# Kernel optimization log

Hardware: AMD Instinct MI355X
Metric: run time of the kernel (lower is better)

## Reference

```python
import jax, jax.numpy as jnp
import numpy as np

PENALTY = -100.0  # reset penalty used by the torch module


def log_g(x):
    # torch: where(x >= 0, log(relu(x) + 0.5), -softplus(-x))
    return jnp.where(x >= 0, jnp.log(jax.nn.relu(x) + 0.5), -jax.nn.softplus(-x))


def setup_inputs() -> dict:
    key = jax.random.key(0)
    k1, k2, k3 = jax.random.split(key, 3)
    B, S, D = 4, 8192, 1024
    x = jax.random.normal(k1, (B, S, D), dtype=jnp.float32)
    W = jax.random.normal(k2, (D, 2 * D), dtype=jnp.float32) * (1.0 / np.sqrt(D))
    input_ids = jax.random.randint(k3, (B, S), 0, 32000, dtype=jnp.int64)
    return {"x": x, "W": W, "input_ids": input_ids}


def reference(x, W, input_ids):
    # x: [B,S,D], W: [D,2D] (to_hidden_and_gate, no bias), proj_out=False -> Identity
    hg = jnp.einsum("bsd,de->bse", x, W)            # [B,S,2D]
    hidden, gate = jnp.split(hg, 2, axis=-1)          # each [B,S,D]

    pad_mask = input_ids == 0                         # [B,S]

    log_coeffs = -jax.nn.softplus(gate)               # log(1 - z)
    log_z = -jax.nn.softplus(-gate)                   # log z
    log_values = log_z + log_g(hidden)                # log(z * h_tilde)

    # reset at positions following a pad token (shifted mask)
    reset = jnp.pad(pad_mask[:, :-1], ((0, 0), (1, 0)))[:, :, None]  # [B,S,1]

    lc = jnp.where(reset, PENALTY, log_coeffs)
    a_star = jnp.cumsum(lc, axis=1)
    lv = jnp.where(reset, PENALTY, log_values)
    log_h = a_star + jax.lax.cumlogsumexp(lv - a_star, axis=1)
    out = jnp.exp(log_h)                              # [B,S,D]

    next_prev_hidden = jnp.where(pad_mask[:, -1:, None], 0.0, out[:, -1:])
    return out, next_prev_hidden
```

## Files before the change

### kernel.cpp

```cpp
#include <hip/hip_runtime.h>
#include <hip/hip_fp16.h>
#include <math.h>

#define S_LEN 8192
#define D_DIM 1024
#define B_DIM 4
#define M_DIM (B_DIM * S_LEN)
#define BSD   ((size_t)M_DIM * D_DIM)
#define CHN   (B_DIM * D_DIM)
#define CHUNK 64
#define NCH   (S_LEN / CHUNK)

typedef _Float16 f16x8 __attribute__((ext_vector_type(8)));
typedef __attribute__((ext_vector_type(4))) float f32x4;
typedef unsigned int u32;

__device__ __forceinline__ u32 pk2h(float a, float b) {
    auto h = __builtin_amdgcn_cvt_pkrtz(a, b);
    u32 r; __builtin_memcpy(&r, &h, 4); return r;
}

__device__ __forceinline__ void gload16(const void* g, void* l) {
    __builtin_amdgcn_global_load_lds(
        (const __attribute__((address_space(1))) u32*)g,
        (__attribute__((address_space(3))) u32*)l,
        16, 0, 0);
}

__global__ __launch_bounds__(256) void w_to_f16t(
    const float* __restrict__ W, unsigned short* __restrict__ Wt)
{
    __shared__ float T[64][65];
    const int t  = threadIdx.x;
    const int n0 = (int)blockIdx.x * 64;
    const int k0 = (int)blockIdx.y * 64;
    #pragma unroll
    for (int p = 0; p < 4; ++p) {
        int u = p * 256 + t;
        int r = u >> 4, c4 = (u & 15) * 4;
        float4 v = *(const float4*)&W[(size_t)(k0 + r) * 2048 + n0 + c4];
        T[r][c4 + 0] = v.x; T[r][c4 + 1] = v.y;
        T[r][c4 + 2] = v.z; T[r][c4 + 3] = v.w;
    }
    __syncthreads();
    #pragma unroll
    for (int p = 0; p < 2; ++p) {
        int u = p * 256 + t;
        int n = u >> 3, kc = (u & 7) * 8;
        u32 out[4];
        #pragma unroll
        for (int j = 0; j < 4; ++j)
            out[j] = pk2h(T[kc + 2 * j][n], T[kc + 2 * j + 1][n]);
        *(uint4*)&Wt[(size_t)(n0 + n) * 1024 + k0 + kc] = *(uint4*)out;
    }
}

__global__ __launch_bounds__(256) void xw_prep(
    const float* __restrict__ x, unsigned short* __restrict__ xh,
    const float* __restrict__ W, unsigned short* __restrict__ Wt)
{
    const int bx = (int)blockIdx.x;
    if (bx < 16384) {
        int tid = bx * 256 + threadIdx.x;
        int m  = tid >> 7;
        int cg = tid & 127;
        const float4* src = (const float4*)&x[(size_t)m * 1024 + cg * 8];
        float4 v0 = src[0], v1 = src[1];
        u32 o[4] = { pk2h(v0.x, v0.y), pk2h(v0.z, v0.w),
                     pk2h(v1.x, v1.y), pk2h(v1.z, v1.w) };
        int j   = cg & 7;
        int cgd = (cg & ~7) | (j ^ (m & 7));
        *(uint4*)&xh[(size_t)m * 1024 + cgd * 8] = *(uint4*)o;
        return;
    }
    __shared__ float T[64][65];
    const int wb = bx - 16384;
    const int t  = threadIdx.x;
    const int n0 = (wb & 31) * 64;
    const int k0 = (wb >> 5) * 64;
    #pragma unroll
    for (int p = 0; p < 4; ++p) {
        int u = p * 256 + t;
        int r = u >> 4, c4 = (u & 15) * 4;
        float4 v = *(const float4*)&W[(size_t)(k0 + r) * 2048 + n0 + c4];
        T[r][c4 + 0] = v.x; T[r][c4 + 1] = v.y;
        T[r][c4 + 2] = v.z; T[r][c4 + 3] = v.w;
    }
    __syncthreads();
    #pragma unroll
    for (int p = 0; p < 2; ++p) {
        int u = p * 256 + t;
        int n = u >> 3, kc = (u & 7) * 8;
        u32 out[4];
        #pragma unroll
        for (int j = 0; j < 4; ++j)
            out[j] = pk2h(T[kc + 2 * j][n], T[kc + 2 * j + 1][n]);
        *(uint4*)&Wt[(size_t)(n0 + n) * 1024 + k0 + kc] = *(uint4*)out;
    }
}

__global__ __launch_bounds__(512, 2) void gemm_8p(
    const unsigned short* __restrict__ xh, const unsigned short* __restrict__ Wt,
    const int* __restrict__ ids, u32* __restrict__ P,
    float* __restrict__ Cp, float* __restrict__ Lp)
{
    __shared__ __align__(16) unsigned short Ah[2 * 256 * 64];
    __shared__ __align__(16) unsigned short Bt[2 * 256 * 64];

    const int t    = threadIdx.x;
    const int lane = t & 63;
    const int wid  = t >> 6;
    const int wm   = wid >> 2;
    const int wd   = wid & 3;

    const int lin  = (int)blockIdx.x;
    const int xcd  = lin & 7;
    const int slot = lin >> 3;
    const int m0   = (xcd * 16 + (slot >> 3)) * 256;
    const int c0   = (slot & 7) * 128;

    f32x4 accH[8][2], accG[8][2];
    #pragma unroll
    for (int i = 0; i < 8; ++i)
        #pragma unroll
        for (int j = 0; j < 2; ++j) {
            accH[i][j] = (f32x4)0.0f;
            accG[i][j] = (f32x4)0.0f;
        }

    auto stageA = [&](int kb, int buf, int half) {
        char* Ad = (char*)Ah + (buf << 15) + (half << 14);
        #pragma unroll
        for (int i = 0; i < 2; ++i) {
            int sl  = i * 512 + t;
            int row = half * 128 + (sl >> 3);
            int c   = sl & 7;
            const unsigned short* src =
                xh + ((size_t)(m0 + row) << 10) + kb + (c << 3);
            gload16(src, Ad + (size_t)sl * 16);
        }
    };
    auto stageB = [&](int kb, int buf, int half) {
        char* Bd = (char*)Bt + (buf << 15) + (half << 14);
        #pragma unroll
        for (int i = 0; i < 2; ++i) {
            int sl  = i * 512 + t;
            int col = sl >> 3;
            int kc  = (sl & 7) ^ (col & 7);
            const unsigned short* src =
                Wt + ((size_t)(half * 1024 + c0 + col) << 10) + kb + (kc << 3);
            gload16(src, Bd + (size_t)sl * 16);
        }
    };

    auto readA = [&](const char* Ab, int kk, f16x8 a[8]) {
        int chunk = kk * 4 + (lane >> 4);
        #pragma unroll
        for (int mf = 0; mf < 8; ++mf) {
            int row = wm * 128 + mf * 16 + (lane & 15);
            a[mf] = *(const f16x8*)(Ab + row * 128 + ((chunk ^ (row & 7)) << 4));
        }
    };
    auto readB = [&](const char* Bb, int kk, int hg, f16x8 b[2]) {
        int chunk = kk * 4 + (lane >> 4);
        #pragma unroll
        for (int df = 0; df < 2; ++df) {
            int col = wd * 32 + df * 16 + (lane & 15);
            b[df] = *(const f16x8*)(Bb + (hg * 128 + col) * 128
                                       + ((chunk ^ (col & 7)) << 4));
        }
    };

    #define MMA_CLUSTER(ACC, AV, BV)                                       \
        __builtin_amdgcn_s_setprio(1);                                     \
        _Pragma("unroll")                                                  \
        for (int mf = 0; mf < 8; ++mf)                                     \
            _Pragma("unroll")                                              \
            for (int df = 0; df < 2; ++df)                                 \
                ACC[mf][df] = __builtin_amdgcn_mfma_f32_16x16x32_f16(      \
                    AV[mf], BV[df], ACC[mf][df], 0, 0, 0);                 \
        __builtin_amdgcn_s_setprio(0);

    stageA(0, 0, 0); stageA(0, 0, 1); stageB(0, 0, 0); stageB(0, 0, 1);
    asm volatile("s_waitcnt vmcnt(0)" ::: "memory");
    __builtin_amdgcn_sched_barrier(0);
    __builtin_amdgcn_s_barrier();

    for (int tt = 0; tt < 16; ++tt) {
        const int buf   = tt & 1;
        const int kbn   = (tt + 1) << 6;
        const bool more = tt < 15;
        const char* Ab = (const char*)Ah + (buf << 15);
        const char* Bb = (const char*)Bt + (buf << 15);
        f16x8 a0[8], a1[8], bh0[2], bg0[2], bh1[2], bg1[2];

        readA(Ab, 0, a0); readB(Bb, 0, 0, bh0);
        if (more) { stageA(kbn, buf ^ 1, 0); stageA(kbn, buf ^ 1, 1); }
        asm volatile("s_waitcnt lgkmcnt(0)" ::: "memory");
        __builtin_amdgcn_sched_barrier(0);
        readB(Bb, 0, 1, bg0);
        __builtin_amdgcn_sched_barrier(0);
        MMA_CLUSTER(accH, a0, bh0)

        asm volatile("s_waitcnt lgkmcnt(0)" ::: "memory");
        __builtin_amdgcn_sched_barrier(0);
        readA(Ab, 1, a1); readB(Bb, 1, 0, bh1);
        if (more) { stageB(kbn, buf ^ 1, 0); stageB(kbn, buf ^ 1, 1); }
        __builtin_amdgcn_sched_barrier(0);
        MMA_CLUSTER(accG, a0, bg0)

        asm volatile("s_waitcnt lgkmcnt(0)" ::: "memory");
        __builtin_amdgcn_sched_barrier(0);
        readB(Bb, 1, 1, bg1);
        __builtin_amdgcn_sched_barrier(0);
        MMA_CLUSTER(accH, a1, bh1)

        asm volatile("s_waitcnt lgkmcnt(0)" ::: "memory");
        __builtin_amdgcn_sched_barrier(0);
        MMA_CLUSTER(accG, a1, bg1)
        if (more) {
            asm volatile("s_waitcnt vmcnt(0)" ::: "memory");
            __builtin_amdgcn_sched_barrier(0);
            __builtin_amdgcn_s_barrier();
        }
    }
    #undef MMA_CLUSTER

    __builtin_amdgcn_s_barrier();
    float* Caff = (float*)Ah;

    #pragma unroll
    for (int mf = 0; mf < 8; ++mf) {
        int mbase = m0 + wm * 128 + mf * 16 + (lane >> 4) * 4;
        float Cr[2] = {1.0f, 1.0f};
        float Lr[2] = {0.0f, 0.0f};
        #pragma unroll
        for (int r = 0; r < 4; ++r) {
            int m = mbase + r;
            int b = m >> 13;
            int s = m & 8191;
            bool reset = (s > 0) && (ids[b * S_LEN + s - 1] == 0);
            #pragma unroll
            for (int df = 0; df < 2; ++df) {
                int d = c0 + wd * 32 + df * 16 + (lane & 15);
                float hid = accH[mf][df][r];
                float g   = accG[mf][df][r];
                float eg  = __expf(-g);
                float z   = 1.0f / (1.0f + eg);
                float c   = eg * z;
                float gt  = (hid >= 0.0f) ? (hid + 0.5f)
                                          : 1.0f / (1.0f + __expf(-hid));
                float v   = z * gt;
                if (reset) { c = 0.0f; v = 0.0f; }
                __half2 h2 = __floats2half2_rn(c, v);
                u32 packed;
                __builtin_memcpy(&packed, &h2, 4);
                P[(size_t)m * D_DIM + d] = packed;
                Lr[df] = fmaf(c, Lr[df], v);
                Cr[df] *= c;
            }
        }
        int rq = wm * 32 + mf * 4 + (lane >> 4);
        #pragma unroll
        for (int df = 0; df < 2; ++df) {
            int col = wd * 32 + df * 16 + (lane & 15);
            Caff[(rq * 128 + col) * 2 + 0] = Cr[df];
            Caff[(rq * 128 + col) * 2 + 1] = Lr[df];
        }
    }
    __builtin_amdgcn_s_barrier();
    {
        int sc  = t >> 7;
        int col = t & 127;
        float C = 1.0f, L = 0.0f;
        #pragma unroll
        for (int q = 0; q < 16; ++q) {
            int rq = sc * 16 + q;
            float cq = Caff[(rq * 128 + col) * 2 + 0];
            float lq = Caff[(rq * 128 + col) * 2 + 1];
            L = fmaf(cq, L, lq);
            C *= cq;
        }
        int m    = m0 + sc * 64;
        int b    = m >> 13;
        int cidx = (m & 8191) >> 6;
        int ch   = (b << 10) | (c0 + col);
        Cp[cidx * CHN + ch] = C;
        Lp[cidx * CHN + ch] = L;
    }
}

__global__ __launch_bounds__(256, 3) void gemm_fb(
    const float* __restrict__ x, const unsigned short* __restrict__ Wt,
    const int* __restrict__ ids, u32* __restrict__ P)
{
    __shared__ __align__(16) unsigned short Ah[128 * 64];
    __shared__ __align__(16) unsigned short Bt[2 * 64 * 64];

    const int t    = threadIdx.x;
    const int lane = t & 63;
    const int wid  = t >> 6;
    const int wm   = wid >> 1;
    const int wd   = wid & 1;

    const int lin  = (int)blockIdx.y * (int)gridDim.x + (int)blockIdx.x;
    const int xcd  = lin & 7;
    const int slot = lin >> 3;
    const int m0   = (xcd * 32 + (slot >> 4)) * 128;
    const int c0   = (slot & 15) * 64;

    f32x4 accH[4][2], accG[4][2];
    #pragma unroll
    for (int i = 0; i < 4; ++i)
        #pragma unroll
        for (int j = 0; j < 2; ++j) {
            accH[i][j] = (f32x4)0.0f;
            accG[i][j] = (f32x4)0.0f;
        }

    for (int kb = 0; kb < 1024; kb += 64) {
        __syncthreads();
        #pragma unroll
        for (int i = 0; i < 4; ++i) {
            int slotb = wid * 256 + i * 64;
            int sl  = slotb + lane;
            int hg  = sl >> 9;
            int col = (sl >> 3) & 63;
            int kc  = (sl & 7) ^ (col & 7);
            const unsigned short* src =
                Wt + ((size_t)(hg * 1024 + c0 + col) << 10) + kb + (kc << 3);
            gload16(src, (char*)Bt + (size_t)slotb * 16);
        }
        #pragma unroll
        for (int p = 0; p < 8; ++p) {
            int s   = p * 256 + t;
            int row = s >> 4;
            int c4  = s & 15;
            float4 v = *(const float4*)&x[(size_t)(m0 + row) * 1024 + kb + c4 * 4];
            uint2 h;
            h.x = pk2h(v.x, v.y);
            h.y = pk2h(v.z, v.w);
            int byte = row * 128 + ((((c4 >> 1) ^ (row & 7))) << 4) + ((c4 & 1) << 3);
            *(uint2*)((char*)Ah + byte) = h;
        }
        __syncthreads();
        #pragma unroll
        for (int kk = 0; kk < 2; ++kk) {
            f16x8 bh[2], bg[2];
            #pragma unroll
            for (int df = 0; df < 2; ++df) {
                int col = wd * 32 + df * 16 + (lane & 15);
                int chunk = kk * 4 + (lane >> 4);
                int byte = col * 128 + ((chunk ^ (col & 7)) << 4);
                bh[df] = *(const f16x8*)((const char*)Bt + byte);
                bg[df] = *(const f16x8*)((const char*)Bt + 8192 + byte);
            }
            #pragma unroll
            for (int mf = 0; mf < 4; ++mf) {
                int row = wm * 64 + mf * 16 + (lane & 15);
                int chunk = kk * 4 + (lane >> 4);
                int byte = row * 128 + ((chunk ^ (row & 7)) << 4);
                f16x8 a = *(const f16x8*)((const char*)Ah + byte);
                #pragma unroll
                for (int df = 0; df < 2; ++df) {
                    accH[mf][df] = __builtin_amdgcn_mfma_f32_16x16x32_f16(
                        a, bh[df], accH[mf][df], 0, 0, 0);
                    accG[mf][df] = __builtin_amdgcn_mfma_f32_16x16x32_f16(
                        a, bg[df], accG[mf][df], 0, 0, 0);
                }
            }
        }
    }

    #pragma unroll
    for (int mf = 0; mf < 4; ++mf) {
        int mbase = m0 + wm * 64 + mf * 16 + (lane >> 4) * 4;
        #pragma unroll
        for (int r = 0; r < 4; ++r) {
            int m = mbase + r;
            int b = m >> 13;
            int s = m & 8191;
            bool reset = (s > 0) && (ids[b * S_LEN + s - 1] == 0);
            #pragma unroll
            for (int df = 0; df < 2; ++df) {
                int d = c0 + wd * 32 + df * 16 + (lane & 15);
                float hid = accH[mf][df][r];
                float g   = accG[mf][df][r];
                float eg  = __expf(-g);
                float z   = 1.0f / (1.0f + eg);
                float c   = eg * z;
                float gt  = (hid >= 0.0f) ? (hid + 0.5f)
                                          : 1.0f / (1.0f + __expf(-hid));
                float v   = z * gt;
                if (reset) { c = 0.0f; v = 0.0f; }
                __half2 h2 = __floats2half2_rn(c, v);
                u32 packed;
                __builtin_memcpy(&packed, &h2, 4);
                P[(size_t)m * D_DIM + d] = packed;
            }
        }
    }
}

__global__ __launch_bounds__(256) void scan_phase_a(
    const u32* __restrict__ P,
    float* __restrict__ Cp, float* __restrict__ Lp)
{
    int ch0 = (blockIdx.x * 256 + threadIdx.x) * 4;
    int c   = blockIdx.y;
    int b   = ch0 >> 10;
    int d0  = ch0 & 1023;
    size_t base = (size_t)b * S_LEN * D_DIM + d0;
    int s0 = c * CHUNK;

    float C[4] = {1.f, 1.f, 1.f, 1.f};
    float H[4] = {0.f, 0.f, 0.f, 0.f};
    for (int s = 0; s < CHUNK; ++s) {
        uint4 q = *(const uint4*)&P[base + (size_t)(s0 + s) * D_DIM];
        u32 qs[4] = {q.x, q.y, q.z, q.w};
        #pragma unroll
        for (int j = 0; j < 4; ++j) {
            __half2 h2;
            __builtin_memcpy(&h2, &qs[j], 4);
            float cc = __low2float(h2);
            float vv = __high2float(h2);
            H[j] = fmaf(cc, H[j], vv);
            C[j] *= cc;
        }
    }
    *(float4*)&Cp[c * CHN + ch0] = *(float4*)C;
    *(float4*)&Lp[c * CHN + ch0] = *(float4*)H;
}

__global__ __launch_bounds__(256) void scan_phase_b(
    const float* __restrict__ Cp, const float* __restrict__ Lp,
    float* __restrict__ carry)
{
    int ch = blockIdx.x * 256 + threadIdx.x;
    float h = 0.0f;
    for (int c = 0; c < NCH; ++c) {
        carry[c * CHN + ch] = h;
        h = fmaf(Cp[c * CHN + ch], h, Lp[c * CHN + ch]);
    }
}

__global__ __launch_bounds__(256) void scan_phase_c(
    u32* __restrict__ Pio,
    const float* __restrict__ carry,
    const int* __restrict__ ids)
{
    int ch0 = (blockIdx.x * 256 + threadIdx.x) * 4;
    int c   = blockIdx.y;
    int b   = ch0 >> 10;
    int d0  = ch0 & 1023;
    size_t base = (size_t)b * S_LEN * D_DIM + d0;
    int s0 = c * CHUNK;

    float H[4];
    *(float4*)H = *(const float4*)&carry[c * CHN + ch0];

    for (int s = 0; s < CHUNK; ++s) {
        size_t idx = base + (size_t)(s0 + s) * D_DIM;
        uint4 q = *(const uint4*)&Pio[idx];
        u32 qs[4] = {q.x, q.y, q.z, q.w};
        u32 os[4];
        #pragma unroll
        for (int j = 0; j < 4; ++j) {
            __half2 h2;
            __builtin_memcpy(&h2, &qs[j], 4);
            float cc = __low2float(h2);
            float vv = __high2float(h2);
            H[j] = fmaf(cc, H[j], vv);
            os[j] = __float_as_uint(H[j]);
        }
        *(uint4*)&Pio[idx] = *(uint4*)os;
    }
    if (c == NCH - 1) {
        bool pad = (ids[b * S_LEN + (S_LEN - 1)] == 0);
        u32 os[4];
        #pragma unroll
        for (int j = 0; j < 4; ++j)
            os[j] = __float_as_uint(pad ? 0.0f : H[j]);
        *(uint4*)&Pio[BSD + (size_t)b * D_DIM + d0] = *(uint4*)os;
    }
}

extern "C" void kernel_launch(void* const* d_in, const int* in_sizes, int n_in,
                              void* d_out, int out_size, void* d_ws, size_t ws_size,
                              hipStream_t stream) {
    const float* x   = (const float*)d_in[0];
    const float* W   = (const float*)d_in[1];
    const int*   ids = (const int*)d_in[2];

    u32* P = (u32*)d_out;
    unsigned short* Wt = (unsigned short*)d_ws;
    float* Cp    = (float*)((char*)d_ws + (size_t) 4 * 1024 * 1024);
    float* Lp    = (float*)((char*)d_ws + (size_t) 6 * 1024 * 1024);
    float* carry = (float*)((char*)d_ws + (size_t) 8 * 1024 * 1024);
    unsigned short* xh = (unsigned short*)((char*)d_ws + (size_t)10 * 1024 * 1024);
    const size_t need = (size_t)10 * 1024 * 1024 + BSD * 2;

    dim3 sgrid(CHN / 1024, NCH);
    if (ws_size >= need) {
        xw_prep<<<16896, 256, 0, stream>>>(x, xh, W, Wt);
        gemm_8p<<<1024, 512, 0, stream>>>(xh, Wt, ids, P, Cp, Lp);
    } else {
        w_to_f16t<<<dim3(32, 16), 256, 0, stream>>>(W, Wt);
        dim3 ggrid(D_DIM / 64, M_DIM / 128);
        gemm_fb<<<ggrid, 256, 0, stream>>>(x, Wt, ids, P);
        scan_phase_a<<<sgrid, 256, 0, stream>>>(P, Cp, Lp);
    }

    scan_phase_b<<<CHN / 256, 256, 0, stream>>>(Cp, Lp, carry);
    scan_phase_c<<<sgrid, 256, 0, stream>>>(P, carry, ids);
}
```

Before: 254.3 us.

## Interleave staged global loads across phases with partial vmcnt waits and barriers

Restructures the K-loop of the GEMM so each of the four MFMA phases issues one stage of next-tile global-to-LDS loads and waits with partial vmcnt counts, instead of waiting for all loads at the end of the iteration. A single B-fragment register array replaces the four separate ones, lowering register pressure. The aim is to spread memory traffic across the iteration and avoid a full drain before each barrier. In exchange it adds several extra workgroup barriers per iteration, and correctness depends on the vmcnt counts matching the loads actually issued.

Measured after the change: 263.2 us. 3.5% more time.

```diff
diff --git a/kernel.cpp b/kernel.cpp
--- a/kernel.cpp
+++ b/kernel.cpp
@@ -192,37 +192,49 @@
         const bool more = tt < 15;
         const char* Ab = (const char*)Ah + (buf << 15);
         const char* Bb = (const char*)Bt + (buf << 15);
-        f16x8 a0[8], a1[8], bh0[2], bg0[2], bh1[2], bg1[2];
-
-        readA(Ab, 0, a0); readB(Bb, 0, 0, bh0);
-        if (more) { stageA(kbn, buf ^ 1, 0); stageA(kbn, buf ^ 1, 1); }
+        f16x8 a0[8], a1[8], b[2];
+
+        readA(Ab, 0, a0);
+        if (more) stageA(kbn, buf ^ 1, 0);
+        if (more) asm volatile("s_waitcnt vmcnt(4)" ::: "memory");
+        else      asm volatile("s_waitcnt vmcnt(2)" ::: "memory");
+        __builtin_amdgcn_sched_barrier(0);
+        __builtin_amdgcn_s_barrier();
+        readB(Bb, 0, 0, b);
         asm volatile("s_waitcnt lgkmcnt(0)" ::: "memory");
         __builtin_amdgcn_sched_barrier(0);
-        readB(Bb, 0, 1, bg0);
-        __builtin_amdgcn_sched_barrier(0);
-        MMA_CLUSTER(accH, a0, bh0)
-
+        MMA_CLUSTER(accH, a0, b)
+        __builtin_amdgcn_s_barrier();
+
+        if (more) stageA(kbn, buf ^ 1, 1);
+        if (more) asm volatile("s_waitcnt vmcnt(4)" ::: "memory");
+        else      asm volatile("s_waitcnt vmcnt(0)" ::: "memory");
+        __builtin_amdgcn_sched_barrier(0);
+        __builtin_amdgcn_s_barrier();
+        readB(Bb, 0, 1, b);
         asm volatile("s_waitcnt lgkmcnt(0)" ::: "memory");
         __builtin_amdgcn_sched_barrier(0);
-        readA(Ab, 1, a1); readB(Bb, 1, 0, bh1);
-        if (more) { stageB(kbn, buf ^ 1, 0); stageB(kbn, buf ^ 1, 1); }
-        __builtin_amdgcn_sched_barrier(0);
-        MMA_CLUSTER(accG, a0, bg0)
-
+        MMA_CLUSTER(accG, a0, b)
+        __builtin_amdgcn_s_barrier();
+
+        readA(Ab, 1, a1);
+        if (more) stageB(kbn, buf ^ 1, 0);
+        __builtin_amdgcn_s_barrier();
+        readB(Bb, 1, 0, b);
         asm volatile("s_waitcnt lgkmcnt(0)" ::: "memory");
         __builtin_amdgcn_sched_barrier(0);
-        readB(Bb, 1, 1, bg1);
-        __builtin_amdgcn_sched_barrier(0);
-        MMA_CLUSTER(accH, a1, bh1)
-
+        MMA_CLUSTER(accH, a1, b)
+        __builtin_amdgcn_s_barrier();
+
+        if (more) stageB(kbn, buf ^ 1, 1);
+        __builtin_amdgcn_s_barrier();
+        readB(Bb, 1, 1, b);
         asm volatile("s_waitcnt lgkmcnt(0)" ::: "memory");
         __builtin_amdgcn_sched_barrier(0);
-        MMA_CLUSTER(accG, a1, bg1)
-        if (more) {
-            asm volatile("s_waitcnt vmcnt(0)" ::: "memory");
-            __builtin_amdgcn_sched_barrier(0);
-            __builtin_amdgcn_s_barrier();
-        }
+        MMA_CLUSTER(accG, a1, b)
+        if (more) asm volatile("s_waitcnt vmcnt(4)" ::: "memory");
+        __builtin_amdgcn_sched_barrier(0);
+        __builtin_amdgcn_s_barrier();
     }
     #undef MMA_CLUSTER
 
```

## Shrink GEMM block tile to 128x64 with 4 waves and remap XCD grid

Applied to the files above, without the earlier changes.

Replaces the 8-wave 256-row by 128-column (times hidden and gate) GEMM block with a 4-wave 128-row by 64-column block launched on four times as many blocks. The block-to-XCD mapping changes so that each XCD owns a set of output columns instead of a set of rows. The intent is to raise occupancy and improve load balance and L2 locality of the W tiles. The cost is less data reuse per block, meaning more global and LDS traffic per FLOP, and more blocks to schedule.

Result: slower. 323.1 us (+27.1%).

```diff
diff --git a/kernel.cpp b/kernel.cpp
--- a/kernel.cpp
+++ b/kernel.cpp
@@ -99,65 +99,66 @@
     }
 }
 
-__global__ __launch_bounds__(512, 2) void gemm_8p(
+__global__ __launch_bounds__(256, 2) void gemm_dc2(
     const unsigned short* __restrict__ xh, const unsigned short* __restrict__ Wt,
     const int* __restrict__ ids, u32* __restrict__ P,
     float* __restrict__ Cp, float* __restrict__ Lp)
 {
-    __shared__ __align__(16) unsigned short Ah[2 * 256 * 64];
-    __shared__ __align__(16) unsigned short Bt[2 * 256 * 64];
+    __shared__ __align__(16) unsigned short Ah[2 * 128 * 64];
+    __shared__ __align__(16) unsigned short Bt[2 * 128 * 64];
 
     const int t    = threadIdx.x;
     const int lane = t & 63;
     const int wid  = t >> 6;
-    const int wm   = wid >> 2;
-    const int wd   = wid & 3;
+    const int wm   = wid >> 1;
+    const int wd   = wid & 1;
 
     const int lin  = (int)blockIdx.x;
     const int xcd  = lin & 7;
     const int slot = lin >> 3;
-    const int m0   = (xcd * 16 + (slot >> 3)) * 256;
-    const int c0   = (slot & 7) * 128;
-
-    f32x4 accH[8][2], accG[8][2];
-    #pragma unroll
-    for (int i = 0; i < 8; ++i)
+    const int m0   = (slot & 255) * 128;
+    const int c0   = (((slot >> 8) << 3) | xcd) * 64;
+
+    f32x4 accH[4][2], accG[4][2];
+    #pragma unroll
+    for (int i = 0; i < 4; ++i)
         #pragma unroll
         for (int j = 0; j < 2; ++j) {
             accH[i][j] = (f32x4)0.0f;
             accG[i][j] = (f32x4)0.0f;
         }
 
-    auto stageA = [&](int kb, int buf, int half) {
-        char* Ad = (char*)Ah + (buf << 15) + (half << 14);
-        #pragma unroll
-        for (int i = 0; i < 2; ++i) {
-            int sl  = i * 512 + t;
-            int row = half * 128 + (sl >> 3);
+    auto stageA = [&](int kb, int buf) {
+        char* Ad = (char*)Ah + (buf << 14);
+        #pragma unroll
+        for (int i = 0; i < 4; ++i) {
+            int sl  = i * 256 + t;
+            int row = sl >> 3;
             int c   = sl & 7;
             const unsigned short* src =
                 xh + ((size_t)(m0 + row) << 10) + kb + (c << 3);
             gload16(src, Ad + (size_t)sl * 16);
         }
     };
-    auto stageB = [&](int kb, int buf, int half) {
-        char* Bd = (char*)Bt + (buf << 15) + (half << 14);
-        #pragma unroll
-        for (int i = 0; i < 2; ++i) {
-            int sl  = i * 512 + t;
+    auto stageB = [&](int kb, int buf) {
+        char* Bd = (char*)Bt + (buf << 14);
+        #pragma unroll
+        for (int i = 0; i < 4; ++i) {
+            int sl  = i * 256 + t;
             int col = sl >> 3;
+            int hg  = col >> 6;
             int kc  = (sl & 7) ^ (col & 7);
             const unsigned short* src =
-                Wt + ((size_t)(half * 1024 + c0 + col) << 10) + kb + (kc << 3);
+                Wt + ((size_t)(hg * 1024 + c0 + (col & 63)) << 10) + kb + (kc << 3);
             gload16(src, Bd + (size_t)sl * 16);
         }
     };
 
-    auto readA = [&](const char* Ab, int kk, f16x8 a[8]) {
+    auto readA = [&](const char* Ab, int kk, f16x8 a[4]) {
         int chunk = kk * 4 + (lane >> 4);
         #pragma unroll
-        for (int mf = 0; mf < 8; ++mf) {
-            int row = wm * 128 + mf * 16 + (lane & 15);
+        for (int mf = 0; mf < 4; ++mf) {
+            int row = wm * 64 + mf * 16 + (lane & 15);
             a[mf] = *(const f16x8*)(Ab + row * 128 + ((chunk ^ (row & 7)) << 4));
         }
     };
@@ -165,23 +166,22 @@
         int chunk = kk * 4 + (lane >> 4);
         #pragma unroll
         for (int df = 0; df < 2; ++df) {
-            int col = wd * 32 + df * 16 + (lane & 15);
-            b[df] = *(const f16x8*)(Bb + (hg * 128 + col) * 128
-                                       + ((chunk ^ (col & 7)) << 4));
+            int col = hg * 64 + wd * 32 + df * 16 + (lane & 15);
+            b[df] = *(const f16x8*)(Bb + col * 128 + ((chunk ^ (col & 7)) << 4));
         }
     };
 
     #define MMA_CLUSTER(ACC, AV, BV)                                       \
         __builtin_amdgcn_s_setprio(1);                                     \
         _Pragma("unroll")                                                  \
-        for (int mf = 0; mf < 8; ++mf)                                     \
+        for (int mf = 0; mf < 4; ++mf)                                     \
             _Pragma("unroll")                                              \
             for (int df = 0; df < 2; ++df)                                 \
                 ACC[mf][df] = __builtin_amdgcn_mfma_f32_16x16x32_f16(      \
                     AV[mf], BV[df], ACC[mf][df], 0, 0, 0);                 \
         __builtin_amdgcn_s_setprio(0);
 
-    stageA(0, 0, 0); stageA(0, 0, 1); stageB(0, 0, 0); stageB(0, 0, 1);
+    stageA(0, 0); stageB(0, 0);
     asm volatile("s_waitcnt vmcnt(0)" ::: "memory");
     __builtin_amdgcn_sched_barrier(0);
     __builtin_amdgcn_s_barrier();
@@ -190,12 +190,12 @@
         const int buf   = tt & 1;
         const int kbn   = (tt + 1) << 6;
         const bool more = tt < 15;
-        const char* Ab = (const char*)Ah + (buf << 15);
-        const char* Bb = (const char*)Bt + (buf << 15);
-        f16x8 a0[8], a1[8], bh0[2], bg0[2], bh1[2], bg1[2];
+        const char* Ab = (const char*)Ah + (buf << 14);
+        const char* Bb = (const char*)Bt + (buf << 14);
+        f16x8 a0[4], a1[4], bh0[2], bg0[2], bh1[2], bg1[2];
 
         readA(Ab, 0, a0); readB(Bb, 0, 0, bh0);
-        if (more) { stageA(kbn, buf ^ 1, 0); stageA(kbn, buf ^ 1, 1); }
+        if (more) stageA(kbn, buf ^ 1);
         asm volatile("s_waitcnt lgkmcnt(0)" ::: "memory");
         __builtin_amdgcn_sched_barrier(0);
         readB(Bb, 0, 1, bg0);
@@ -205,7 +205,7 @@
         asm volatile("s_waitcnt lgkmcnt(0)" ::: "memory");
         __builtin_amdgcn_sched_barrier(0);
         readA(Ab, 1, a1); readB(Bb, 1, 0, bh1);
-        if (more) { stageB(kbn, buf ^ 1, 0); stageB(kbn, buf ^ 1, 1); }
+        if (more) stageB(kbn, buf ^ 1);
         __builtin_amdgcn_sched_barrier(0);
         MMA_CLUSTER(accG, a0, bg0)
 
@@ -230,8 +230,8 @@
     float* Caff = (float*)Ah;
 
     #pragma unroll
-    for (int mf = 0; mf < 8; ++mf) {
-        int mbase = m0 + wm * 128 + mf * 16 + (lane >> 4) * 4;
+    for (int mf = 0; mf < 4; ++mf) {
+        int mbase = m0 + wm * 64 + mf * 16 + (lane >> 4) * 4;
         float Cr[2] = {1.0f, 1.0f};
         float Lr[2] = {0.0f, 0.0f};
         #pragma unroll
@@ -260,24 +260,23 @@
                 Cr[df] *= c;
             }
         }
-        int rq = wm * 32 + mf * 4 + (lane >> 4);
+        int rq = mf * 4 + (lane >> 4);
         #pragma unroll
         for (int df = 0; df < 2; ++df) {
             int col = wd * 32 + df * 16 + (lane & 15);
-            Caff[(rq * 128 + col) * 2 + 0] = Cr[df];
-            Caff[(rq * 128 + col) * 2 + 1] = Lr[df];
+            Caff[((wm * 16 + rq) * 64 + col) * 2 + 0] = Cr[df];
+            Caff[((wm * 16 + rq) * 64 + col) * 2 + 1] = Lr[df];
         }
     }
     __builtin_amdgcn_s_barrier();
-    {
-        int sc  = t >> 7;
-        int col = t & 127;
+    if (t < 128) {
+        int sc  = t >> 6;
+        int col = t & 63;
         float C = 1.0f, L = 0.0f;
         #pragma unroll
         for (int q = 0; q < 16; ++q) {
-            int rq = sc * 16 + q;
-            float cq = Caff[(rq * 128 + col) * 2 + 0];
-            float lq = Caff[(rq * 128 + col) * 2 + 1];
+            float cq = Caff[((sc * 16 + q) * 64 + col) * 2 + 0];
+            float lq = Caff[((sc * 16 + q) * 64 + col) * 2 + 1];
             L = fmaf(cq, L, lq);
             C *= cq;
         }
@@ -503,7 +502,7 @@
     dim3 sgrid(CHN / 1024, NCH);
     if (ws_size >= need) {
         xw_prep<<<16896, 256, 0, stream>>>(x, xh, W, Wt);
-        gemm_8p<<<1024, 512, 0, stream>>>(xh, Wt, ids, P, Cp, Lp);
+        gemm_dc2<<<4096, 256, 0, stream>>>(xh, Wt, ids, P, Cp, Lp);
     } else {
         w_to_f16t<<<dim3(32, 16), 256, 0, stream>>>(W, Wt);
         dim3 ggrid(D_DIM / 64, M_DIM / 128);
```
